# Performance work log

Measured on AMD Instinct MI355X. Metric: run time of the kernel, lower is better.

The kernel has to match this reference:

```python
import jax, jax.numpy as jnp
import numpy as np

M, N, D = 2048, 131072, 256

def setup_inputs() -> dict:
    key = jax.random.key(0)
    kq, kv = jax.random.split(key)
    query = jax.random.normal(kq, (M, D), dtype=jnp.float32)
    vectors = jax.random.normal(kv, (N, D), dtype=jnp.float32)
    return {"query": query, "vectors": vectors}

def reference(query, vectors):
    # torch.cdist(query, vectors, p=2).argmin(dim=1)
    # Euclidean distance via ||q||^2 + ||v||^2 - 2 q.v (GEMM-based, same math)
    q_sq = jnp.sum(query * query, axis=-1, keepdims=True)        # [M,1]
    v_sq = jnp.sum(vectors * vectors, axis=-1)                    # [N]
    cross = jnp.einsum('md,nd->mn', query, vectors)               # [M,N]
    dist_sq = jnp.maximum(q_sq + v_sq[None, :] - 2.0 * cross, 0.0)
    # sqrt is monotonic so argmin(dist) == argmin(dist_sq); take sqrt for faithfulness
    dist = jnp.sqrt(dist_sq)
    return jnp.argmin(dist, axis=1)                               # [M] int
```

## Files before the change

kernel.cpp:

```cpp
#include <hip/hip_runtime.h>
#include <hip/hip_bf16.h>

#define M 2048
#define N 131072
#define D 256

#define SLICE_G 64
#define NSLICE  (N / (SLICE_G * 16))
#define BIAS    1024.0f

typedef __attribute__((ext_vector_type(8))) _Float16 half8;
typedef __attribute__((ext_vector_type(8))) short short8;
typedef __attribute__((ext_vector_type(4))) float f32x4;
typedef unsigned long long ull;

__device__ __forceinline__ ull pack_key(float score, unsigned idx) {
    unsigned u = __float_as_uint(score);
    u = (u & 0x80000000u) ? ~u : (u | 0x80000000u);
    return ((ull)u << 32) | idx;
}

__global__ __launch_bounds__(256) void convert_fused(const float* __restrict__ v,
                                                     const float* __restrict__ q,
                                                     short* __restrict__ vf,
                                                     short* __restrict__ qf,
                                                     float* __restrict__ vsqb,
                                                     ull* __restrict__ keys) {
    __shared__ float part[4][16];
    const int b    = blockIdx.x;
    const bool isV = (b < N / 16);
    const int g    = isV ? b : (b - N / 16);
    const float* x = isV ? v : q;
    short* xf      = isV ? vf : qf;

    const int t    = threadIdx.x;
    const int w    = t >> 6;
    const int l    = t & 63;
    const int quad = (t >> 4) & 3;
    const int tx   = t & 15;

    float s = 0.f;
#pragma unroll
    for (int h = 0; h < 2; ++h) {
        const int c = w + h * 4;
        const float* src = x + (size_t)(g * 16 + tx) * D + c * 32 + quad * 8;
        float tmp[8] __attribute__((aligned(16)));
        *(float4*)&tmp[0] = *(const float4*)src;
        *(float4*)&tmp[4] = *(const float4*)(src + 4);
        half8 hh;
#pragma unroll
        for (int e = 0; e < 8; ++e) {
            hh[e] = (_Float16)tmp[e];
            s += tmp[e] * tmp[e];
        }
        *(short8*)(xf + ((size_t)g * 8 + c) * 512 + l * 8) = *(short8*)&hh;
    }
    if (isV) {
        s += __shfl_xor(s, 16, 64);
        s += __shfl_xor(s, 32, 64);
        if (l < 16) part[w][l] = s;
        __syncthreads();
        if (t < 16) vsqb[g * 16 + t] = part[0][t] + part[1][t] + part[2][t] + part[3][t] + BIAS;
    } else if (g == 0) {
        for (int i = t; i < 2 * M; i += 256) keys[i] = ~0ull;
    }
}

__global__ __launch_bounds__(256) void dist_argmin_reg(const short* __restrict__ qf,
                                                       const short* __restrict__ vf,
                                                       const float* __restrict__ vsqb,
                                                       ull* __restrict__ keys1,
                                                       ull* __restrict__ keys2) {
    const int tid  = threadIdx.x;
    const int lane = tid & 63;
    const int w    = tid >> 6;
    const int tx   = lane & 15;
    const int quad = (lane >> 4) & 3;

    const int lb    = blockIdx.x;
    const int xcd   = lb & 7;
    const int s_    = lb >> 3;
    const int slice = xcd * (NSLICE / 8) + (s_ >> 4);
    const int qblk  = s_ & 15;

    const int qb0 = qblk * 128 + w * 32;
    const int sg0 = slice * SLICE_G;

    half8 aq[2][8];
#pragma unroll
    for (int mt = 0; mt < 2; ++mt)
#pragma unroll
        for (int c = 0; c < 8; ++c)
            aq[mt][c] = *(const half8*)(qf + ((size_t)((qb0 >> 4) + mt) * 8 + c) * 512 + lane * 8);

    unsigned best[8];
#pragma unroll
    for (int i = 0; i < 8; ++i) best[i] = 0xFFFFFFFFu;

    const short* bp = vf + ((size_t)sg0 * 8) * 512 + lane * 8;
    const float* vp = vsqb + sg0 * 16 + tx;

    half8 bA[8], bB[8];
    float vA, vB;

    auto loadg = [&](half8* b, float& vs, int g) {
        const short* p = bp + (size_t)g * 4096;
#pragma unroll
        for (int c = 0; c < 8; ++c) b[c] = *(const half8*)(p + c * 512);
        vs = vp[g * 16];
    };
    auto compute = [&](const half8* b, float vsqr, int g) {
        f32x4 acc[2][2];
#pragma unroll
        for (int i = 0; i < 2; ++i) {
            acc[i][0] = (f32x4){0.f, 0.f, 0.f, 0.f};
            acc[i][1] = (f32x4){0.f, 0.f, 0.f, 0.f};
        }
#pragma unroll
        for (int c = 0; c < 8; ++c) {
            acc[0][c & 1] = __builtin_amdgcn_mfma_f32_16x16x32_f16(aq[0][c], b[c], acc[0][c & 1], 0, 0, 0);
            acc[1][c & 1] = __builtin_amdgcn_mfma_f32_16x16x32_f16(aq[1][c], b[c], acc[1][c & 1], 0, 0, 0);
        }
#pragma unroll
        for (int mt = 0; mt < 2; ++mt)
#pragma unroll
            for (int r = 0; r < 4; ++r) {
                const float sc = fmaf(-2.f, acc[mt][0][r], fmaf(-2.f, acc[mt][1][r], vsqr));
                const unsigned key = (__float_as_uint(sc) & 0xFFFFFFC0u) | (unsigned)g;
                const int sl = mt * 4 + r;
                best[sl] = key < best[sl] ? key : best[sl];
            }
    };

    loadg(bA, vA, 0);
    for (int g = 0; g < SLICE_G - 2; g += 2) {
        loadg(bB, vB, g + 1);
        compute(bA, vA, g);
        loadg(bA, vA, g + 2);
        compute(bB, vB, g + 1);
    }
    loadg(bB, vB, SLICE_G - 1);
    compute(bA, vA, SLICE_G - 2);
    compute(bB, vB, SLICE_G - 1);

#pragma unroll
    for (int mt = 0; mt < 2; ++mt)
#pragma unroll
        for (int r = 0; r < 4; ++r) {
            const int sl = mt * 4 + r;
            unsigned k = best[sl];
#pragma unroll
            for (int off = 8; off; off >>= 1) {
                const unsigned o = (unsigned)__shfl_xor((int)k, off, 16);
                k = o < k ? o : k;
            }
            const ull bal = __ballot(best[sl] == k);
            const unsigned grp = (unsigned)((bal >> (quad * 16)) & 0xFFFFull);
            const int wtx = __ffs((int)grp) - 1;
            const unsigned n = (unsigned)((sg0 + (int)(k & 63u)) * 16 + wtx);
            if (tx == 0) {
                const int row = qb0 + mt * 16 + quad * 4 + r;
                const ull key64 = ((ull)k << 32) | n;
                const ull old = atomicMin(&keys1[row], key64);
                const ull loser = (key64 < old) ? old : key64;
                if (loser != ~0ull) atomicMin(&keys2[row], loser);
            }
        }
}

__global__ __launch_bounds__(256) void rescore_kernel(const float* __restrict__ q,
                                                      const float* __restrict__ v,
                                                      const ull* __restrict__ keys1,
                                                      const ull* __restrict__ keys2,
                                                      int* __restrict__ out) {
    const int qi   = blockIdx.x * 4 + (threadIdx.x >> 6);
    const int lane = threadIdx.x & 63;
    const float4 qv = *(const float4*)(q + (size_t)qi * D + lane * 4);
    ull best = ~0ull;
    ull cand[2];
    cand[0] = keys1[qi];
    cand[1] = keys2[qi];
#pragma unroll
    for (int c = 0; c < 2; ++c) {
        if (cand[c] == ~0ull) continue;
        const unsigned idx = (unsigned)cand[c];
        const float4 vv = *(const float4*)(v + (size_t)idx * D + lane * 4);
        float s1 = vv.x * vv.x + vv.y * vv.y + vv.z * vv.z + vv.w * vv.w;
        float s2 = qv.x * vv.x + qv.y * vv.y + qv.z * vv.z + qv.w * vv.w;
#pragma unroll
        for (int off = 32; off; off >>= 1) {
            s1 += __shfl_xor(s1, off, 64);
            s2 += __shfl_xor(s2, off, 64);
        }
        const float dist = fmaf(-2.0f, s2, s1);
        const ull key = pack_key(dist, idx);
        best = best < key ? best : key;
    }
    if (lane == 0) out[qi] = (int)(unsigned)(best & 0xFFFFFFFFull);
}

extern "C" void kernel_launch(void* const* d_in, const int* in_sizes, int n_in,
                              void* d_out, int out_size, void* d_ws, size_t ws_size,
                              hipStream_t stream) {
    const float* q = (const float*)d_in[0];
    const float* v = (const float*)d_in[1];
    int* out = (int*)d_out;

    char* ws = (char*)d_ws;
    float* vsqb = (float*)ws;                ws += (size_t)N * sizeof(float);
    ull* keys1 = (ull*)ws;                   ws += (size_t)2 * M * sizeof(ull);
    ull* keys2 = keys1 + M;
    short* qf = (short*)ws;                  ws += (size_t)M * D * 2;
    short* vf = (short*)ws;

    convert_fused<<<N / 16 + M / 16, 256, 0, stream>>>(v, q, vf, qf, vsqb, keys1);

    dist_argmin_reg<<<16 * NSLICE, 256, 0, stream>>>(qf, vf, vsqb, keys1, keys2);

    rescore_kernel<<<M / 4, 256, 0, stream>>>(q, v, keys1, keys2, out);
}
```

Baseline: 355.1 us.

## Double per-wave query tile to 64 rows and stage conversion loads through LDS

The distance kernel now gives each wave 64 query rows instead of 32, so each block covers 256 queries. Every loaded vector tile feeds twice as many MFMAs, which halves the global traffic over the 128 MB fp16 vector set, and the grid shrinks accordingly. The split dual accumulators are merged into a single accumulator chain, and launch_bounds(256,2) is added to cap register use. The conversion kernel now does coalesced float4 loads into padded LDS before converting, replacing the strided row reads. The risks are much higher register pressure from 32 query fragments plus 16 best slots, and longer dependent MFMA chains.

```diff
diff --git a/kernel.cpp b/kernel.cpp
--- a/kernel.cpp
+++ b/kernel.cpp
@@ -26,7 +26,9 @@
                                                      short* __restrict__ qf,
                                                      float* __restrict__ vsqb,
                                                      ull* __restrict__ keys) {
+    __shared__ float lds[16 * 260];
     __shared__ float part[4][16];
+
     const int b    = blockIdx.x;
     const bool isV = (b < N / 16);
     const int g    = isV ? b : (b - N / 16);
@@ -36,17 +38,27 @@
     const int t    = threadIdx.x;
     const int w    = t >> 6;
     const int l    = t & 63;
-    const int quad = (t >> 4) & 3;
-    const int tx   = t & 15;
+    const int quad = (l >> 4) & 3;
+    const int tx   = l & 15;
+
+    const float* src = x + (size_t)g * 4096;
+#pragma unroll
+    for (int i = 0; i < 4; ++i) {
+        const int fi  = (i * 256 + t) * 4;
+        const float4 f = *(const float4*)(src + fi);
+        const int row = fi >> 8;
+        const int col = fi & 255;
+        *(float4*)&lds[row * 260 + col] = f;
+    }
+    __syncthreads();
 
     float s = 0.f;
 #pragma unroll
     for (int h = 0; h < 2; ++h) {
         const int c = w + h * 4;
-        const float* src = x + (size_t)(g * 16 + tx) * D + c * 32 + quad * 8;
         float tmp[8] __attribute__((aligned(16)));
-        *(float4*)&tmp[0] = *(const float4*)src;
-        *(float4*)&tmp[4] = *(const float4*)(src + 4);
+        *(float4*)&tmp[0] = *(const float4*)&lds[tx * 260 + c * 32 + quad * 8];
+        *(float4*)&tmp[4] = *(const float4*)&lds[tx * 260 + c * 32 + quad * 8 + 4];
         half8 hh;
 #pragma unroll
         for (int e = 0; e < 8; ++e) {
@@ -55,6 +67,7 @@
         }
         *(short8*)(xf + ((size_t)g * 8 + c) * 512 + l * 8) = *(short8*)&hh;
     }
+
     if (isV) {
         s += __shfl_xor(s, 16, 64);
         s += __shfl_xor(s, 32, 64);
@@ -66,11 +79,11 @@
     }
 }
 
-__global__ __launch_bounds__(256) void dist_argmin_reg(const short* __restrict__ qf,
-                                                       const short* __restrict__ vf,
-                                                       const float* __restrict__ vsqb,
-                                                       ull* __restrict__ keys1,
-                                                       ull* __restrict__ keys2) {
+__global__ __launch_bounds__(256, 2) void dist_argmin_reg(const short* __restrict__ qf,
+                                                          const short* __restrict__ vf,
+                                                          const float* __restrict__ vsqb,
+                                                          ull* __restrict__ keys1,
+                                                          ull* __restrict__ keys2) {
     const int tid  = threadIdx.x;
     const int lane = tid & 63;
     const int w    = tid >> 6;
@@ -80,22 +93,22 @@
     const int lb    = blockIdx.x;
     const int xcd   = lb & 7;
     const int s_    = lb >> 3;
-    const int slice = xcd * (NSLICE / 8) + (s_ >> 4);
-    const int qblk  = s_ & 15;
-
-    const int qb0 = qblk * 128 + w * 32;
+    const int slice = xcd * 16 + (s_ >> 3);
+    const int qblk  = s_ & 7;
+
+    const int qb0 = qblk * 256 + w * 64;
     const int sg0 = slice * SLICE_G;
 
-    half8 aq[2][8];
-#pragma unroll
-    for (int mt = 0; mt < 2; ++mt)
+    half8 aq[4][8];
+#pragma unroll
+    for (int mt = 0; mt < 4; ++mt)
 #pragma unroll
         for (int c = 0; c < 8; ++c)
             aq[mt][c] = *(const half8*)(qf + ((size_t)((qb0 >> 4) + mt) * 8 + c) * 512 + lane * 8);
 
-    unsigned best[8];
-#pragma unroll
-    for (int i = 0; i < 8; ++i) best[i] = 0xFFFFFFFFu;
+    unsigned best[16];
+#pragma unroll
+    for (int i = 0; i < 16; ++i) best[i] = 0xFFFFFFFFu;
 
     const short* bp = vf + ((size_t)sg0 * 8) * 512 + lane * 8;
     const float* vp = vsqb + sg0 * 16 + tx;
@@ -110,22 +123,19 @@
         vs = vp[g * 16];
     };
     auto compute = [&](const half8* b, float vsqr, int g) {
-        f32x4 acc[2][2];
-#pragma unroll
-        for (int i = 0; i < 2; ++i) {
-            acc[i][0] = (f32x4){0.f, 0.f, 0.f, 0.f};
-            acc[i][1] = (f32x4){0.f, 0.f, 0.f, 0.f};
-        }
-#pragma unroll
-        for (int c = 0; c < 8; ++c) {
-            acc[0][c & 1] = __builtin_amdgcn_mfma_f32_16x16x32_f16(aq[0][c], b[c], acc[0][c & 1], 0, 0, 0);
-            acc[1][c & 1] = __builtin_amdgcn_mfma_f32_16x16x32_f16(aq[1][c], b[c], acc[1][c & 1], 0, 0, 0);
-        }
-#pragma unroll
-        for (int mt = 0; mt < 2; ++mt)
+        f32x4 acc[4];
+#pragma unroll
+        for (int i = 0; i < 4; ++i) acc[i] = (f32x4){0.f, 0.f, 0.f, 0.f};
+#pragma unroll
+        for (int c = 0; c < 8; ++c)
+#pragma unroll
+            for (int mt = 0; mt < 4; ++mt)
+                acc[mt] = __builtin_amdgcn_mfma_f32_16x16x32_f16(aq[mt][c], b[c], acc[mt], 0, 0, 0);
+#pragma unroll
+        for (int mt = 0; mt < 4; ++mt)
 #pragma unroll
             for (int r = 0; r < 4; ++r) {
-                const float sc = fmaf(-2.f, acc[mt][0][r], fmaf(-2.f, acc[mt][1][r], vsqr));
+                const float sc = fmaf(-2.f, acc[mt][r], vsqr);
                 const unsigned key = (__float_as_uint(sc) & 0xFFFFFFC0u) | (unsigned)g;
                 const int sl = mt * 4 + r;
                 best[sl] = key < best[sl] ? key : best[sl];
@@ -144,7 +154,7 @@
     compute(bB, vB, SLICE_G - 1);
 
 #pragma unroll
-    for (int mt = 0; mt < 2; ++mt)
+    for (int mt = 0; mt < 4; ++mt)
 #pragma unroll
         for (int r = 0; r < 4; ++r) {
             const int sl = mt * 4 + r;
@@ -215,7 +225,7 @@
 
     convert_fused<<<N / 16 + M / 16, 256, 0, stream>>>(v, q, vf, qf, vsqb, keys1);
 
-    dist_argmin_reg<<<16 * NSLICE, 256, 0, stream>>>(qf, vf, vsqb, keys1, keys2);
+    dist_argmin_reg<<<(M / 256) * NSLICE, 256, 0, stream>>>(qf, vf, vsqb, keys1, keys2);
 
     rescore_kernel<<<M / 4, 256, 0, stream>>>(q, v, keys1, keys2, out);
 }
```

Result: faster. 321.5 us (-9.5%).

## Stage loads through LDS and process two vector groups per MFMA step

Applied to the files above, without the earlier changes.

The convert kernel now copies each 16-row tile into LDS with coalesced float4 loads and builds the fp16 fragments from LDS, where before each thread gathered strided rows from global memory. The distance kernel first stages the block's query tile into a 64KB LDS buffer, then loads A fragments from there. It also processes two 16-vector groups per step with independent accumulators, so each group's dot product runs as one accumulation chain. This doubles the B register buffers and adds launch_bounds(256,2), which raises register pressure and may cause spills or lower occupancy.

```diff
diff --git a/kernel.cpp b/kernel.cpp
--- a/kernel.cpp
+++ b/kernel.cpp
@@ -6,6 +6,7 @@
 #define D 256
 
 #define SLICE_G 64
+#define NWG     (SLICE_G / 2)
 #define NSLICE  (N / (SLICE_G * 16))
 #define BIAS    1024.0f
 
@@ -26,7 +27,9 @@
                                                      short* __restrict__ qf,
                                                      float* __restrict__ vsqb,
                                                      ull* __restrict__ keys) {
+    __shared__ float lds[16 * 260];
     __shared__ float part[4][16];
+
     const int b    = blockIdx.x;
     const bool isV = (b < N / 16);
     const int g    = isV ? b : (b - N / 16);
@@ -36,17 +39,27 @@
     const int t    = threadIdx.x;
     const int w    = t >> 6;
     const int l    = t & 63;
-    const int quad = (t >> 4) & 3;
-    const int tx   = t & 15;
+    const int quad = (l >> 4) & 3;
+    const int tx   = l & 15;
+
+    const float* src = x + (size_t)g * 4096;
+#pragma unroll
+    for (int i = 0; i < 4; ++i) {
+        const int fi  = (i * 256 + t) * 4;
+        const float4 f = *(const float4*)(src + fi);
+        const int row = fi >> 8;
+        const int col = fi & 255;
+        *(float4*)&lds[row * 260 + col] = f;
+    }
+    __syncthreads();
 
     float s = 0.f;
 #pragma unroll
     for (int h = 0; h < 2; ++h) {
         const int c = w + h * 4;
-        const float* src = x + (size_t)(g * 16 + tx) * D + c * 32 + quad * 8;
         float tmp[8] __attribute__((aligned(16)));
-        *(float4*)&tmp[0] = *(const float4*)src;
-        *(float4*)&tmp[4] = *(const float4*)(src + 4);
+        *(float4*)&tmp[0] = *(const float4*)&lds[tx * 260 + c * 32 + quad * 8];
+        *(float4*)&tmp[4] = *(const float4*)&lds[tx * 260 + c * 32 + quad * 8 + 4];
         half8 hh;
 #pragma unroll
         for (int e = 0; e < 8; ++e) {
@@ -55,6 +68,7 @@
         }
         *(short8*)(xf + ((size_t)g * 8 + c) * 512 + l * 8) = *(short8*)&hh;
     }
+
     if (isV) {
         s += __shfl_xor(s, 16, 64);
         s += __shfl_xor(s, 32, 64);
@@ -66,11 +80,13 @@
     }
 }
 
-__global__ __launch_bounds__(256) void dist_argmin_reg(const short* __restrict__ qf,
-                                                       const short* __restrict__ vf,
-                                                       const float* __restrict__ vsqb,
-                                                       ull* __restrict__ keys1,
-                                                       ull* __restrict__ keys2) {
+__global__ __launch_bounds__(256, 2) void dist_argmin_reg(const short* __restrict__ qf,
+                                                          const short* __restrict__ vf,
+                                                          const float* __restrict__ vsqb,
+                                                          ull* __restrict__ keys1,
+                                                          ull* __restrict__ keys2) {
+    __shared__ __align__(16) short sA[128 * 256];
+
     const int tid  = threadIdx.x;
     const int lane = tid & 63;
     const int w    = tid >> 6;
@@ -80,18 +96,28 @@
     const int lb    = blockIdx.x;
     const int xcd   = lb & 7;
     const int s_    = lb >> 3;
-    const int slice = xcd * (NSLICE / 8) + (s_ >> 4);
+    const int slice = xcd * 16 + (s_ >> 4);
     const int qblk  = s_ & 15;
 
     const int qb0 = qblk * 128 + w * 32;
     const int sg0 = slice * SLICE_G;
 
+    {
+        const short* qsrc = qf + (size_t)qblk * 32768;
+#pragma unroll
+        for (int i = 0; i < 16; ++i) {
+            const int off = (i * 256 + tid) * 8;
+            *(short8*)(sA + off) = *(const short8*)(qsrc + off);
+        }
+    }
+    __syncthreads();
+
     half8 aq[2][8];
 #pragma unroll
     for (int mt = 0; mt < 2; ++mt)
 #pragma unroll
         for (int c = 0; c < 8; ++c)
-            aq[mt][c] = *(const half8*)(qf + ((size_t)((qb0 >> 4) + mt) * 8 + c) * 512 + lane * 8);
+            aq[mt][c] = *(const half8*)(sA + ((2 * w + mt) * 8 + c) * 512 + lane * 8);
 
     unsigned best[8];
 #pragma unroll
@@ -100,16 +126,20 @@
     const short* bp = vf + ((size_t)sg0 * 8) * 512 + lane * 8;
     const float* vp = vsqb + sg0 * 16 + tx;
 
-    half8 bA[8], bB[8];
-    float vA, vB;
-
-    auto loadg = [&](half8* b, float& vs, int g) {
-        const short* p = bp + (size_t)g * 4096;
-#pragma unroll
-        for (int c = 0; c < 8; ++c) b[c] = *(const half8*)(p + c * 512);
-        vs = vp[g * 16];
+    half8 bA[16], bB[16];
+    float vA0, vA1, vB0, vB1;
+
+    auto loadwg = [&](half8* b, float& v0, float& v1, int wg) {
+        const short* p = bp + (size_t)wg * 8192;
+#pragma unroll
+        for (int c = 0; c < 8; ++c) {
+            b[c]     = *(const half8*)(p + c * 512);
+            b[8 + c] = *(const half8*)(p + 4096 + c * 512);
+        }
+        v0 = vp[(2 * wg) * 16];
+        v1 = vp[(2 * wg + 1) * 16];
     };
-    auto compute = [&](const half8* b, float vsqr, int g) {
+    auto compute = [&](const half8* b, float v0, float v1, int wg) {
         f32x4 acc[2][2];
 #pragma unroll
         for (int i = 0; i < 2; ++i) {
@@ -117,31 +147,36 @@
             acc[i][1] = (f32x4){0.f, 0.f, 0.f, 0.f};
         }
 #pragma unroll
-        for (int c = 0; c < 8; ++c) {
-            acc[0][c & 1] = __builtin_amdgcn_mfma_f32_16x16x32_f16(aq[0][c], b[c], acc[0][c & 1], 0, 0, 0);
-            acc[1][c & 1] = __builtin_amdgcn_mfma_f32_16x16x32_f16(aq[1][c], b[c], acc[1][c & 1], 0, 0, 0);
-        }
+        for (int c = 0; c < 8; ++c)
+#pragma unroll
+            for (int mt = 0; mt < 2; ++mt) {
+                acc[mt][0] = __builtin_amdgcn_mfma_f32_16x16x32_f16(aq[mt][c], b[c],     acc[mt][0], 0, 0, 0);
+                acc[mt][1] = __builtin_amdgcn_mfma_f32_16x16x32_f16(aq[mt][c], b[8 + c], acc[mt][1], 0, 0, 0);
+            }
 #pragma unroll
         for (int mt = 0; mt < 2; ++mt)
 #pragma unroll
             for (int r = 0; r < 4; ++r) {
-                const float sc = fmaf(-2.f, acc[mt][0][r], fmaf(-2.f, acc[mt][1][r], vsqr));
-                const unsigned key = (__float_as_uint(sc) & 0xFFFFFFC0u) | (unsigned)g;
+                const float s0 = fmaf(-2.f, acc[mt][0][r], v0);
+                const float s1 = fmaf(-2.f, acc[mt][1][r], v1);
+                const unsigned k0 = (__float_as_uint(s0) & 0xFFFFFFC0u) | (unsigned)(2 * wg);
+                const unsigned k1 = (__float_as_uint(s1) & 0xFFFFFFC0u) | (unsigned)(2 * wg + 1);
                 const int sl = mt * 4 + r;
-                best[sl] = key < best[sl] ? key : best[sl];
+                unsigned m = k0 < k1 ? k0 : k1;
+                best[sl] = m < best[sl] ? m : best[sl];
             }
     };
 
-    loadg(bA, vA, 0);
-    for (int g = 0; g < SLICE_G - 2; g += 2) {
-        loadg(bB, vB, g + 1);
-        compute(bA, vA, g);
-        loadg(bA, vA, g + 2);
-        compute(bB, vB, g + 1);
-    }
-    loadg(bB, vB, SLICE_G - 1);
-    compute(bA, vA, SLICE_G - 2);
-    compute(bB, vB, SLICE_G - 1);
+    loadwg(bA, vA0, vA1, 0);
+    for (int wg = 0; wg < NWG - 2; wg += 2) {
+        loadwg(bB, vB0, vB1, wg + 1);
+        compute(bA, vA0, vA1, wg);
+        loadwg(bA, vA0, vA1, wg + 2);
+        compute(bB, vB0, vB1, wg + 1);
+    }
+    loadwg(bB, vB0, vB1, NWG - 1);
+    compute(bA, vA0, vA1, NWG - 2);
+    compute(bB, vB0, vB1, NWG - 1);
 
 #pragma unroll
     for (int mt = 0; mt < 2; ++mt)
@@ -215,7 +250,7 @@
 
     convert_fused<<<N / 16 + M / 16, 256, 0, stream>>>(v, q, vf, qf, vsqb, keys1);
 
-    dist_argmin_reg<<<16 * NSLICE, 256, 0, stream>>>(qf, vf, vsqb, keys1, keys2);
+    dist_argmin_reg<<<(M / 128) * NSLICE, 256, 0, stream>>>(qf, vf, vsqb, keys1, keys2);
 
     rescore_kernel<<<M / 4, 256, 0, stream>>>(q, v, keys1, keys2, out);
 }
```

Result: no change. 353.8 us (-0.4%).
